# Performance work log

Measured on AMD Instinct MI355X. Metric: run time of the kernel, lower is better.

Reference implementation:

```python
import jax, jax.numpy as jnp
import numpy as np
from jax import lax

B, T, C, H, W = 1, 6, 64, 128, 128
DG, K = 16, 9          # deformable groups, 3x3 kernel positions
CG = C // DG
MRM = 10.0             # max_residue_magnitude


def _conv3(x, w, b):
    y = lax.conv_general_dilated(x, w, (1, 1), 'SAME',
                                 dimension_numbers=('NCHW', 'OIHW', 'NCHW'))
    return y + b[None, :, None, None]


def _leaky(x):
    return jnp.where(x >= 0, x, 0.1 * x)


def _bilinear(img, py, px):
    # img [N,Cc,h,w]; py/px [N,*S] unnormalized pixel coords; zero padding outside.
    N, Cc, h, w = img.shape
    S = py.shape[1:]
    py = py.reshape(N, -1)
    px = px.reshape(N, -1)
    y0 = jnp.floor(py); x0 = jnp.floor(px)
    fy = py - y0; fx = px - x0
    y0 = y0.astype(jnp.int32); x0 = x0.astype(jnp.int32)
    imf = img.reshape(N, Cc, h * w)

    def corner(yi, xi, wt):
        valid = (yi >= 0) & (yi < h) & (xi >= 0) & (xi < w)
        idx = jnp.clip(yi, 0, h - 1) * w + jnp.clip(xi, 0, w - 1)
        v = jax.vmap(lambda im, ix: im[:, ix])(imf, idx)  # [N,Cc,M]
        return v * (wt * valid)[:, None, :]

    out = (corner(y0, x0, (1 - fy) * (1 - fx))
           + corner(y0, x0 + 1, (1 - fy) * fx)
           + corner(y0 + 1, x0, fy * (1 - fx))
           + corner(y0 + 1, x0 + 1, fy * fx))
    return out.reshape(N, Cc, *S)


def _flow_warp(x, flow):
    # flow [N,2,H,W]: channel 0 = x-displacement, channel 1 = y-displacement
    gy = jnp.arange(H, dtype=jnp.float32)
    gx = jnp.arange(W, dtype=jnp.float32)
    py = gy[None, :, None] + flow[:, 1]
    px = gx[None, None, :] + flow[:, 0]
    return _bilinear(x, py, px)


def _mod_deform_conv(x, offset, mask, w, b):
    # offset [N, 2*DG*K, H, W] interleaved (y,x) per (group, kernel pos); mask [N, DG*K, H, W]
    N = x.shape[0]
    off = offset.reshape(N, DG, K, 2, H, W)
    kh = (jnp.arange(K) // 3).astype(jnp.float32)
    kw = (jnp.arange(K) % 3).astype(jnp.float32)
    gy = jnp.arange(H, dtype=jnp.float32)
    gx = jnp.arange(W, dtype=jnp.float32)
    # stride 1, padding 1, dilation 1, 3x3 kernel
    py = gy[None, None, None, :, None] - 1.0 + kh[None, None, :, None, None] + off[:, :, :, 0]
    px = gx[None, None, None, None, :] - 1.0 + kw[None, None, :, None, None] + off[:, :, :, 1]
    xg = x.reshape(N, DG, CG, H, W).reshape(N * DG, CG, H, W)
    s = _bilinear(xg, py.reshape(N * DG, K, H, W), px.reshape(N * DG, K, H, W))
    s = s.reshape(N, DG, CG, K, H, W) * mask.reshape(N, DG, 1, K, H, W)
    wr = w.reshape(C, DG, CG, K)
    return jnp.einsum('ngckhw,ogck->nohw', s, wr) + b[None, :, None, None]


def setup_inputs() -> dict:
    key = jax.random.key(0)
    ks = jax.random.split(key, 10)
    rn = lambda k, s, sc: jax.random.normal(k, s, jnp.float32) * sc
    cin = 2 * C + 2  # (1 + n_frames//2)*C + n_frames
    return {
        'x': rn(ks[0], (B, T, C, H, W), 1.0),
        'flows_backward': rn(ks[1], (B, T - 1, 2, H, W), 2.0),
        'flows_forward': rn(ks[2], (B, T - 1, 2, H, W), 2.0),
        'cw1': rn(ks[3], (C, cin, 3, 3), 1.0 / np.sqrt(cin * 9)),
        'cb1': jnp.zeros((C,), jnp.float32),
        'cw2': rn(ks[4], (C, C, 3, 3), 1.0 / np.sqrt(C * 9)),
        'cb2': jnp.zeros((C,), jnp.float32),
        'cw3': rn(ks[5], (C, C, 3, 3), 1.0 / np.sqrt(C * 9)),
        'cb3': jnp.zeros((C,), jnp.float32),
        # original zero-inits the last conv; use small random so offsets/masks are nontrivial
        'cw4': rn(ks[6], (3 * K * DG, C, 3, 3), 0.01),
        'cb4': jnp.zeros((3 * K * DG,), jnp.float32),
        'dcn_w': rn(ks[7], (C, C, 3, 3), 1.0 / np.sqrt(C * 9)),
        'dcn_b': jnp.zeros((C,), jnp.float32),
    }


def reference(x, flows_backward, flows_forward, cw1, cb1, cw2, cb2, cw3, cb3,
              cw4, cb4, dcn_w, dcn_b):
    # Batch all backward-pass frame pairs (i=T-1..1) and forward-pass pairs (i=0..T-2)
    # into one effective batch of B*2*(T-1) independent DCN calls.
    xi = jnp.concatenate([x[:, 1:], x[:, :-1]], axis=1)      # source frames
    cur = jnp.concatenate([x[:, :-1], x[:, 1:]], axis=1)     # target (current) frames
    fl = jnp.concatenate([flows_backward, flows_forward], axis=1)
    N = B * 2 * (T - 1)
    xi = xi.reshape(N, C, H, W)
    cur = cur.reshape(N, C, H, W)
    fl = fl.reshape(N, 2, H, W)

    warped = _flow_warp(xi, fl)
    inp = jnp.concatenate([warped, cur, fl], axis=1)          # [N, 2C+2, H, W]
    h1 = _leaky(_conv3(inp, cw1, cb1))
    h2 = _leaky(_conv3(h1, cw2, cb2))
    h3 = _leaky(_conv3(h2, cw3, cb3))
    out = _conv3(h3, cw4, cb4)                                # [N, 3*9*DG, H, W]
    o1, o2, m = jnp.split(out, 3, axis=1)
    offset = MRM * jnp.tanh(jnp.concatenate([o1, o2], axis=1))
    # flow.flip(1).repeat -> interleaved (fy, fx) added to every (group, kernel pos)
    offset = offset + jnp.tile(fl[:, ::-1], (1, DG * K, 1, 1))
    mask = jax.nn.sigmoid(m)

    feat = _mod_deform_conv(xi, offset, mask, dcn_w, dcn_b)   # [N, C, H, W]
    feat = feat.reshape(B, 2, T - 1, C, H, W)
    zeros = jnp.zeros((B, 1, C, H, W), feat.dtype)
    x_backward = jnp.concatenate([feat[:, 0], zeros], axis=1)  # [B, T, C, H, W]
    x_forward = jnp.concatenate([zeros, feat[:, 1]], axis=1)   # [B, T, C, H, W]
    return x_backward, x_forward
```

## Files before the change

kernel.cpp:

```cpp
#include <hip/hip_runtime.h>
#include <math.h>

#define NP   10
#define C_   64
#define H_   128
#define W_   128
#define HW   (H_*W_)
#define MRM_ 10.0f

#define OMB8_OFF 23040u
#define LDS8_TOT 30720

#define W1T_N 82944
#define W2T_N 36864
#define W4_N  294912
#define DWT_N 49152

typedef __bf16 bf16x8 __attribute__((ext_vector_type(8)));
typedef float  f32x16 __attribute__((ext_vector_type(16)));

#define MEM_FENCE() do { asm volatile("" ::: "memory"); \
                         __builtin_amdgcn_sched_barrier(0); } while (0)

__device__ __forceinline__ f32x16 mfma32(bf16x8 a, bf16x8 b, f32x16 c) {
    return __builtin_amdgcn_mfma_f32_32x32x16_bf16(a, b, c, 0, 0, 0);
}

__device__ __forceinline__ ushort bfrn(float f) {
    uint u = __builtin_bit_cast(uint, f);
    u += 0x7FFFu + ((u >> 16) & 1u);
    return (ushort)(u >> 16);
}
__device__ __forceinline__ float blo(uint u) { return __builtin_bit_cast(float, u << 16); }
__device__ __forceinline__ float bhi(uint u) { return __builtin_bit_cast(float, u & 0xFFFF0000u); }
__device__ __forceinline__ float fast_tanh(float x) {
    float e = __expf(2.f * x);
    return 1.f - 2.f / (e + 1.f);
}

__device__ __forceinline__ const float* xi_base(const float* x, int n) {
    int f = (n < 5) ? (n + 1) : (n - 5);
    return x + (size_t)f * C_ * HW;
}
__device__ __forceinline__ const float* cur_base(const float* x, int n) {
    int f = (n < 5) ? n : (n - 4);
    return x + (size_t)f * C_ * HW;
}
__device__ __forceinline__ const float* fl_base(const float* fb, const float* ff, int n) {
    return (n < 5) ? (fb + (size_t)n * 2 * HW) : (ff + (size_t)(n - 5) * 2 * HW);
}

struct Bil { int i00, i01, i10, i11; float m00, m01, m10, m11; };
__device__ __forceinline__ Bil bil(float py, float px) {
    float y0f = floorf(py), x0f = floorf(px);
    int iy0 = (int)y0f, ix0 = (int)x0f;
    float ay = py - y0f, ax = px - x0f;
    bool v0y = (unsigned)iy0 < (unsigned)H_;
    bool v1y = (unsigned)(iy0 + 1) < (unsigned)H_;
    bool v0x = (unsigned)ix0 < (unsigned)W_;
    bool v1x = (unsigned)(ix0 + 1) < (unsigned)W_;
    int cy0 = min(max(iy0, 0), H_ - 1), cy1 = min(max(iy0 + 1, 0), H_ - 1);
    int cx0 = min(max(ix0, 0), W_ - 1), cx1 = min(max(ix0 + 1, 0), W_ - 1);
    Bil r;
    r.m00 = (1.f - ay) * (1.f - ax) * (float)(v0y && v0x);
    r.m01 = (1.f - ay) * ax         * (float)(v0y && v1x);
    r.m10 = ay * (1.f - ax)         * (float)(v1y && v0x);
    r.m11 = ay * ax                 * (float)(v1y && v1x);
    r.i00 = cy0 * W_ + cx0; r.i01 = cy0 * W_ + cx1;
    r.i10 = cy1 * W_ + cx0; r.i11 = cy1 * W_ + cx1;
    return r;
}

__global__ __launch_bounds__(256) void k_prep(
        const float* __restrict__ cw1, const float* __restrict__ cw2,
        const float* __restrict__ cw3, const float* __restrict__ cw4,
        const float* __restrict__ cb4, const float* __restrict__ dw,
        ushort* __restrict__ w1t, ushort* __restrict__ w2t,
        ushort* __restrict__ w3t, ushort* __restrict__ w4t,
        ushort* __restrict__ dwtb, float* __restrict__ pb4) {
    int id = blockIdx.x * 256 + threadIdx.x;
    if (id < W1T_N) {
        int blk = id >> 9, e = id & 511;
        int c = blk / 18, r = blk % 18; int t = r >> 1, nf = r & 1;
        int l = e >> 3, j = e & 7;
        int ci = c * 16 + (l >> 5) * 8 + j;
        int oc = nf * 32 + (l & 31);
        w1t[id] = (ci < 130) ? bfrn(cw1[((size_t)oc * 130 + ci) * 9 + t]) : (ushort)0;
        return;
    }
    id -= W1T_N;
    if (id < W2T_N) {
        int blk = id >> 9, e = id & 511;
        int c = blk / 18, r = blk % 18; int t = r >> 1, nf = r & 1;
        int l = e >> 3, j = e & 7;
        int ci = c * 16 + (l >> 5) * 8 + j;
        int oc = nf * 32 + (l & 31);
        w2t[id] = bfrn(cw2[((size_t)oc * 64 + ci) * 9 + t]);
        return;
    }
    id -= W2T_N;
    if (id < W2T_N) {
        int blk = id >> 9, e = id & 511;
        int c = blk / 18, r = blk % 18; int t = r >> 1, nf = r & 1;
        int l = e >> 3, j = e & 7;
        int ci = c * 16 + (l >> 5) * 8 + j;
        int oc = nf * 32 + (l & 31);
        w3t[id] = bfrn(cw3[((size_t)oc * 64 + ci) * 9 + t]);
        return;
    }
    id -= W2T_N;
    if (id < W4_N) {
        int blk = id >> 9, e = id & 511;
        int c = blk / 144, r = blk - c * 144;
        int t = r >> 4, g = r & 15;
        int l = e >> 3, j = e & 7;
        int nn = l & 31, kh = l >> 5;
        int ci = c * 16 + kh * 8 + j;
        int ch = (nn < 18) ? g * 18 + nn : (nn < 27 ? 288 + g * 9 + (nn - 18) : -1);
        float v = (ch >= 0) ? cw4[((size_t)ch * 64 + ci) * 9 + t] : 0.f;
        w4t[id] = bfrn(v);
        return;
    }
    id -= W4_N;
    if (id < DWT_N) {
        int blk = id >> 9, e = id & 511;
        int g = blk / 6, r = blk - g * 6;
        int kst = r >> 1, nf = r & 1;
        int l = e >> 3, j = e & 7;
        int kk = kst * 16 + (l >> 5) * 8 + j;
        int oc = nf * 32 + (l & 31);
        float v = (kk < 36) ? dw[((size_t)oc * 64 + g * 4 + (kk & 3)) * 9 + (kk >> 2)] : 0.f;
        dwtb[id] = bfrn(v);
        return;
    }
    id -= DWT_N;
    if (id < 512) {
        int g = id >> 5, nn = id & 31;
        int ch = (nn < 18) ? g * 18 + nn : (nn < 27 ? 288 + g * 9 + (nn - 18) : -1);
        pb4[id] = (ch >= 0) ? cb4[ch] : 0.f;
    }
}

__global__ __launch_bounds__(256) void k_warp(
        const float* __restrict__ x, const float* __restrict__ fb,
        const float* __restrict__ ff, ushort* __restrict__ warped) {
    int gid = blockIdx.x * 256 + threadIdx.x;
    int n = gid / HW, pos = gid % HW;
    int y = pos / W_, xx = pos % W_;
    const float* fl = fl_base(fb, ff, n);
    float fx = fl[pos], fy = fl[HW + pos];
    Bil b = bil((float)y + fy, (float)xx + fx);
    const float* xb = xi_base(x, n);
    ushort* wout = warped + (size_t)n * C_ * HW + pos;
    for (int c = 0; c < C_; ++c) {
        const float* p = xb + c * HW;
        wout[c * HW] = bfrn(b.m00 * p[b.i00] + b.m01 * p[b.i01]
                          + b.m10 * p[b.i10] + b.m11 * p[b.i11]);
    }
}

__global__ __launch_bounds__(256) void k_xt(
        const float* __restrict__ x, ushort* __restrict__ xt) {
    int gid = blockIdx.x * 256 + threadIdx.x;
    int f = gid / HW, pos = gid % HW;
    const float* src = x + (size_t)f * C_ * HW + pos;
    ushort* dst = xt + (size_t)f * 16 * HW * 4;
    #pragma unroll
    for (int g = 0; g < 16; ++g) {
        uint2 v;
        ushort h0 = bfrn(src[(g * 4 + 0) * HW]);
        ushort h1 = bfrn(src[(g * 4 + 1) * HW]);
        ushort h2 = bfrn(src[(g * 4 + 2) * HW]);
        ushort h3 = bfrn(src[(g * 4 + 3) * HW]);
        v.x = (uint)h0 | ((uint)h1 << 16);
        v.y = (uint)h2 | ((uint)h3 << 16);
        *(uint2*)(dst + ((size_t)g * HW + pos) * 4) = v;
    }
}

template<int NCHUNK, int SRC>
__global__ __launch_bounds__(256, 3) void k_convm(
        const ushort* __restrict__ inb, const float* __restrict__ x,
        const float* __restrict__ fb, const float* __restrict__ ff,
        const ushort* __restrict__ wt, const float* __restrict__ bias,
        ushort* __restrict__ outp) {
    __shared__ __align__(16) char ldsb[41472];
    int tid = threadIdx.x;
    int lane = tid & 63, w = tid >> 6;
    int id = (blockIdx.x & 7) * 80 + (blockIdx.x >> 3);
    int bx = id & 7, by = (id >> 3) & 7, n = id >> 6;
    int col = lane & 31, khalf = lane >> 5;

    const float* flp = fl_base(fb, ff, n);
    const float* curp = cur_base(x, n);

    f32x16 acc[2][2];
    #pragma unroll
    for (int a = 0; a < 2; ++a)
        #pragma unroll
        for (int b = 0; b < 2; ++b)
            #pragma unroll
            for (int r = 0; r < 16; ++r) acc[a][b][r] = 0.f;

    int xb2 = col & 15;
    int rb0 = 4 * w + ((col >> 4) & 1);
    const int NPASS = (NCHUNK + 3) / 4;

    #pragma unroll
    for (int p = 0; p < NPASS; ++p) {
        const int c0 = 4 * p;
        const int cN = (NCHUNK - c0 >= 4) ? 4 : (NCHUNK - c0);
        __syncthreads();
        for (int cc = 0; cc < cN; ++cc) {
            int chunk = c0 + cc;
            int cbase = chunk * 16 + w * 4;
            for (int v = 0; v < 6; ++v) {
                int cell = v * 64 + lane;
                if (cell < 324) {
                    int cy = cell / 18, cx = cell - cy * 18;
                    int gy = by * 16 + cy - 1, gx = bx * 16 + cx - 1;
                    bool ok = ((unsigned)gy < 128u) && ((unsigned)gx < 128u);
                    int pos = gy * W_ + gx;
                    uint2 hv; hv.x = hv.y = 0;
                    if (SRC == 1 || chunk < 4) {
                        const ushort* sp = inb + ((size_t)n * 64 + cbase) * HW + pos;
                        ushort h0 = ok ? sp[0] : (ushort)0;
                        ushort h1 = ok ? sp[HW] : (ushort)0;
                        ushort h2 = ok ? sp[2 * HW] : (ushort)0;
                        ushort h3 = ok ? sp[3 * HW] : (ushort)0;
                        hv.x = (uint)h0 | ((uint)h1 << 16);
                        hv.y = (uint)h2 | ((uint)h3 << 16);
                    } else if (chunk < 8) {
                        const float* sp = curp + (size_t)(cbase - 64) * HW + pos;
                        ushort h0 = bfrn(ok ? sp[0] : 0.f);
                        ushort h1 = bfrn(ok ? sp[HW] : 0.f);
                        ushort h2 = bfrn(ok ? sp[2 * HW] : 0.f);
                        ushort h3 = bfrn(ok ? sp[3 * HW] : 0.f);
                        hv.x = (uint)h0 | ((uint)h1 << 16);
                        hv.y = (uint)h2 | ((uint)h3 << 16);
                    } else {
                        float v0 = 0.f, v1 = 0.f;
                        if (w == 0 && ok) { v0 = flp[pos]; v1 = flp[HW + pos]; }
                        hv.x = (uint)bfrn(v0) | ((uint)bfrn(v1) << 16);
                    }
                    uint byte = (uint)cell * 128 + (uint)cc * 32 + (uint)w * 8;
                    byte ^= ((uint)(cell & 7)) << 4;
                    *(uint2*)(ldsb + byte) = hv;
                }
            }
        }
        __syncthreads();
        for (int cc = 0; cc < cN; ++cc) {
            #pragma unroll
            for (int t = 0; t < 9; ++t) {
                const int ky = t / 3, kx = t % 3;
                size_t bb = (size_t)(((c0 + cc) * 9 + t) * 2) * 512 + (size_t)lane * 8;
                bf16x8 b0 = *(const bf16x8*)(wt + bb);
                bf16x8 b1 = *(const bf16x8*)(wt + bb + 512);
                #pragma unroll
                for (int f = 0; f < 2; ++f) {
                    int cell = (rb0 + 2 * f + ky) * 18 + xb2 + kx;
                    uint byte = (uint)cell * 128 + (uint)(2 * cc + khalf) * 16;
                    byte ^= ((uint)(cell & 7)) << 4;
                    bf16x8 a = *(const bf16x8*)(ldsb + byte);
                    acc[f][0] = mfma32(a, b0, acc[f][0]);
                    acc[f][1] = mfma32(a, b1, acc[f][1]);
                }
            }
        }
    }

    ushort* op = outp + (size_t)n * 64 * HW;
    #pragma unroll
    for (int f = 0; f < 2; ++f)
        #pragma unroll
        for (int nf = 0; nf < 2; ++nf) {
            int oc = nf * 32 + col;
            float bs = bias[oc];
            #pragma unroll
            for (int r = 0; r < 16; ++r) {
                int pxl = 64 * w + 32 * f + (r & 3) + 8 * (r >> 2) + 4 * khalf;
                int y = by * 16 + (pxl >> 4), xx = bx * 16 + (pxl & 15);
                float v = acc[f][nf][r] + bs;
                v = (v >= 0.f) ? v : 0.1f * v;
                op[(size_t)oc * HW + y * W_ + xx] = bfrn(v);
            }
        }
}

__global__ __launch_bounds__(128, 2) void k_dcn11(
        const ushort* __restrict__ h3, const ushort* __restrict__ xt,
        const float* __restrict__ fb, const float* __restrict__ ff,
        const ushort* __restrict__ w4hi,
        const ushort* __restrict__ dwtb, const float* __restrict__ pb4,
        const float* __restrict__ db, float* __restrict__ outb) {
    __shared__ __align__(16) char lds[LDS8_TOT];
    _Float16* OMBH = (_Float16*)(lds + OMB8_OFF);

    int tid = threadIdx.x;
    int lane = tid & 63, w = tid >> 6;
    int id = (blockIdx.x & 7) * 160 + (blockIdx.x >> 3);
    int bx = id & 15, by = (id >> 4) & 7, n = id >> 7;
    int col = lane & 31, khalf = lane >> 5;

    const ushort* h3n = h3 + (size_t)n * 64 * HW;
    const float* fl = fl_base(fb, ff, n);
    int fxi = (n < 5) ? (n + 1) : (n - 5);
    const ushort* xtn = xt + (size_t)fxi * 16 * HW * 4;

    int Yp = by * 16 + (tid >> 3), Xp = bx * 8 + (tid & 7);
    float fxr = fl[Yp * W_ + Xp];
    float fyr = fl[HW + Yp * W_ + Xp];

    for (int c = 0; c < 4; ++c) {
        for (int v = 0; v < 3; ++v) {
            int cell = v * 64 + lane;
            if (cell < 180) {
                int cy = cell / 10, cx = cell - cy * 10;
                int gy = by * 16 + cy - 1, gx = bx * 8 + cx - 1;
                bool ok = ((unsigned)gy < 128u) && ((unsigned)gx < 128u);
                const ushort* srcp = h3n + (size_t)(c * 16 + w * 8) * HW + gy * W_ + gx;
                uint2 hv0, hv1;
                ushort q0 = ok ? srcp[0] : (ushort)0;
                ushort q1 = ok ? srcp[HW] : (ushort)0;
                ushort q2 = ok ? srcp[2 * HW] : (ushort)0;
                ushort q3 = ok ? srcp[3 * HW] : (ushort)0;
                ushort q4 = ok ? srcp[4 * HW] : (ushort)0;
                ushort q5 = ok ? srcp[5 * HW] : (ushort)0;
                ushort q6 = ok ? srcp[6 * HW] : (ushort)0;
                ushort q7 = ok ? srcp[7 * HW] : (ushort)0;
                hv0.x = (uint)q0 | ((uint)q1 << 16);
                hv0.y = (uint)q2 | ((uint)q3 << 16);
                hv1.x = (uint)q4 | ((uint)q5 << 16);
                hv1.y = (uint)q6 | ((uint)q7 << 16);
                uint byte = (uint)cell * 128 + (uint)c * 32 + (uint)w * 16;
                byte ^= ((uint)(cell & 7)) << 4;
                *(uint2*)(lds + byte) = hv0;
                *(uint2*)(lds + byte + 8) = hv1;
            }
        }
    }
    __syncthreads();

    f32x16 zero16;
    #pragma unroll
    for (int r = 0; r < 16; ++r) zero16[r] = 0.f;

    f32x16 cd[2][2];
    #pragma unroll
    for (int a = 0; a < 2; ++a)
        #pragma unroll
        for (int b = 0; b < 2; ++b) cd[a][b] = zero16;

    int colq = col >> 3;
    int colx = col & 7;
    int ad0 = (lane & 31) * 4;

    for (int sp = 0; sp < 8; ++sp) {
        int g0 = sp * 2;
        f32x16 c4[2][2];
        #pragma unroll
        for (int a = 0; a < 2; ++a)
            #pragma unroll
            for (int b = 0; b < 2; ++b) c4[a][b] = zero16;

        __builtin_amdgcn_s_setprio(1);
        #pragma unroll 1
        for (int c = 0; c < 4; ++c) {
            #pragma unroll
            for (int t = 0; t < 9; ++t) {
                const int ky = t / 3, kx = t % 3;
                size_t bb = (size_t)((c * 9 + t) * 16) * 512 + (size_t)lane * 8;
                bf16x8 bh0 = *(const bf16x8*)(w4hi + bb + (size_t)g0 * 512);
                bf16x8 bh1 = *(const bf16x8*)(w4hi + bb + (size_t)(g0 + 1) * 512);
                #pragma unroll
                for (int f = 0; f < 2; ++f) {
                    int cell = (8 * w + 4 * f + colq + ky) * 10 + colx + kx;
                    uint byte = (uint)cell * 128 + (uint)(2 * c + khalf) * 16;
                    byte ^= ((uint)(cell & 7)) << 4;
                    bf16x8 ah = *(const bf16x8*)(lds + byte);
                    c4[0][f] = mfma32(ah, bh0, c4[0][f]);
                    c4[1][f] = mfma32(ah, bh1, c4[1][f]);
                }
            }
        }
        __builtin_amdgcn_s_setprio(0);

        #pragma unroll
        for (int gg = 0; gg < 2; ++gg) {
            int g = g0 + gg;
            MEM_FENCE();
            if (col < 27) {
                float pb = pb4[g * 32 + col];
                #pragma unroll
                for (int f = 0; f < 2; ++f)
                    #pragma unroll
                    for (int r = 0; r < 16; ++r) {
                        int pxl = 64 * w + 32 * f + (r & 3) + 8 * (r >> 2) + 4 * khalf;
                        float v = c4[gg][f][r] + pb;
                        v = (col < 18) ? MRM_ * fast_tanh(v) : 1.f / (1.f + __expf(-v));
                        OMBH[pxl * 30 + col] = (_Float16)v;
                    }
            }
            MEM_FENCE();
            int pkx[9], pky[9];
            {
                int px = tid;
                float Yf = (float)Yp, Xf = (float)Xp;
                const ushort* xg = xtn + (size_t)g * HW * 4;
                #pragma unroll
                for (int k = 0; k < 9; ++k) {
                    float oy = (float)OMBH[px * 30 + 2 * k] + fyr;
                    float ox = (float)OMBH[px * 30 + 2 * k + 1] + fxr;
                    float mk = (float)OMBH[px * 30 + 18 + k];
                    Bil b = bil(Yf - 1.f + (float)(k / 3) + oy,
                                Xf - 1.f + (float)(k % 3) + ox);
                    uint2 q00 = *(const uint2*)(xg + (size_t)b.i00 * 4);
                    uint2 q01 = *(const uint2*)(xg + (size_t)b.i01 * 4);
                    uint2 q10 = *(const uint2*)(xg + (size_t)b.i10 * 4);
                    uint2 q11 = *(const uint2*)(xg + (size_t)b.i11 * 4);
                    float s0 = b.m00 * blo(q00.x) + b.m01 * blo(q01.x)
                             + b.m10 * blo(q10.x) + b.m11 * blo(q11.x);
                    float s1 = b.m00 * bhi(q00.x) + b.m01 * bhi(q01.x)
                             + b.m10 * bhi(q10.x) + b.m11 * bhi(q11.x);
                    float s2 = b.m00 * blo(q00.y) + b.m01 * blo(q01.y)
                             + b.m10 * blo(q10.y) + b.m11 * blo(q11.y);
                    float s3 = b.m00 * bhi(q00.y) + b.m01 * bhi(q01.y)
                             + b.m10 * bhi(q10.y) + b.m11 * bhi(q11.y);
                    pkx[k] = (int)((uint)bfrn(s0 * mk) | ((uint)bfrn(s1 * mk) << 16));
                    pky[k] = (int)((uint)bfrn(s2 * mk) | ((uint)bfrn(s3 * mk) << 16));
                }
            }
            __builtin_amdgcn_s_setprio(1);
            #pragma unroll
            for (int kst = 0; kst < 3; ++kst) {
                size_t dbb = (size_t)((g * 3 + kst) * 2) * 512 + (size_t)lane * 8;
                bf16x8 b0 = *(const bf16x8*)(dwtb + dbb);
                bf16x8 b1 = *(const bf16x8*)(dwtb + dbb + 512);
                #pragma unroll
                for (int f = 0; f < 2; ++f) {
                    int ad = ad0 + f * 128;
                    uint a0, a1, a2, a3;
                    if (kst < 2) {
                        const int t0 = kst * 4;
                        uint x0 = (uint)__builtin_amdgcn_ds_bpermute(ad, pkx[t0]);
                        uint y0 = (uint)__builtin_amdgcn_ds_bpermute(ad, pky[t0]);
                        uint x1 = (uint)__builtin_amdgcn_ds_bpermute(ad, pkx[t0 + 1]);
                        uint y1 = (uint)__builtin_amdgcn_ds_bpermute(ad, pky[t0 + 1]);
                        uint x2 = (uint)__builtin_amdgcn_ds_bpermute(ad, pkx[t0 + 2]);
                        uint y2 = (uint)__builtin_amdgcn_ds_bpermute(ad, pky[t0 + 2]);
                        uint x3 = (uint)__builtin_amdgcn_ds_bpermute(ad, pkx[t0 + 3]);
                        uint y3 = (uint)__builtin_amdgcn_ds_bpermute(ad, pky[t0 + 3]);
                        a0 = khalf ? x2 : x0;
                        a1 = khalf ? y2 : y0;
                        a2 = khalf ? x3 : x1;
                        a3 = khalf ? y3 : y1;
                    } else {
                        uint x8 = (uint)__builtin_amdgcn_ds_bpermute(ad, pkx[8]);
                        uint y8 = (uint)__builtin_amdgcn_ds_bpermute(ad, pky[8]);
                        a0 = khalf ? 0u : x8;
                        a1 = khalf ? 0u : y8;
                        a2 = 0u; a3 = 0u;
                    }
                    uint4 av; av.x = a0; av.y = a1; av.z = a2; av.w = a3;
                    bf16x8 a = __builtin_bit_cast(bf16x8, av);
                    cd[f][0] = mfma32(a, b0, cd[f][0]);
                    cd[f][1] = mfma32(a, b1, cd[f][1]);
                }
            }
            __builtin_amdgcn_s_setprio(0);
        }
    }

    float* base = (n < 5) ? outb + (size_t)n * 64 * HW
                          : outb + (size_t)(n + 2) * 64 * HW;
    #pragma unroll
    for (int f = 0; f < 2; ++f)
        #pragma unroll
        for (int nf = 0; nf < 2; ++nf) {
            int oc = nf * 32 + col;
            float bias = db[oc];
            #pragma unroll
            for (int r = 0; r < 16; ++r) {
                int pxl = 64 * w + 32 * f + (r & 3) + 8 * (r >> 2) + 4 * khalf;
                int y = by * 16 + (pxl >> 3), xx = bx * 8 + (pxl & 7);
                base[(size_t)oc * HW + y * W_ + xx] = cd[f][nf][r] + bias;
            }
        }
}

extern "C" void kernel_launch(void* const* d_in, const int* in_sizes, int n_in,
                              void* d_out, int out_size, void* d_ws, size_t ws_size,
                              hipStream_t stream) {
    (void)in_sizes; (void)n_in; (void)out_size; (void)ws_size;
    const float* x   = (const float*)d_in[0];
    const float* fb  = (const float*)d_in[1];
    const float* ff  = (const float*)d_in[2];
    const float* cw1 = (const float*)d_in[3];
    const float* cb1 = (const float*)d_in[4];
    const float* cw2 = (const float*)d_in[5];
    const float* cb2 = (const float*)d_in[6];
    const float* cw3 = (const float*)d_in[7];
    const float* cb3 = (const float*)d_in[8];
    const float* cw4 = (const float*)d_in[9];
    const float* cb4 = (const float*)d_in[10];
    const float* dw  = (const float*)d_in[11];
    const float* db  = (const float*)d_in[12];
    float* out = (float*)d_out;

    ushort* h1b  = (ushort*)d_ws;
    ushort* h3b  = h1b + 10485760;
    ushort* w1t  = h3b + 10485760;
    ushort* w2t  = w1t + W1T_N;
    ushort* w3t  = w2t + W2T_N;
    ushort* w4t  = w3t + W2T_N;
    ushort* dwtb = w4t + W4_N;
    float*  pb4  = (float*)(dwtb + DWT_N);
    ushort* xtb  = h1b;
    ushort* wpb  = (ushort*)d_out;
    ushort* h2b  = wpb + 10485760;

    k_prep<<<1958, 256, 0, stream>>>(cw1, cw2, cw3, cw4, cb4, dw,
                                     w1t, w2t, w3t, w4t, dwtb, pb4);
    k_warp<<<(NP * HW) / 256, 256, 0, stream>>>(x, fb, ff, wpb);
    k_convm<9, 0><<<640, 256, 0, stream>>>(wpb, x, fb, ff, w1t, cb1, h1b);
    k_convm<4, 1><<<640, 256, 0, stream>>>(h1b, x, fb, ff, w2t, cb2, h2b);
    k_xt<<<(6 * HW) / 256, 256, 0, stream>>>(x, xtb);
    k_convm<4, 1><<<640, 256, 0, stream>>>(h2b, x, fb, ff, w3t, cb3, h3b);

    hipMemsetAsync((char*)d_out + (size_t)5 * C_ * HW * sizeof(float), 0, (size_t)C_ * HW * sizeof(float), stream);
    hipMemsetAsync((char*)d_out + (size_t)6 * C_ * HW * sizeof(float), 0, (size_t)C_ * HW * sizeof(float), stream);

    k_dcn11<<<1280, 128, 0, stream>>>(h3b, xtb, fb, ff, w4t, dwtb, pb4, db, out);
}
```

Before: 604.1 us.

## Halve DCN tile to 8x8 pixels per block, split bilinear taps across half-waves

The fused offset-conv plus deformable-conv kernel now processes an 8x8 pixel tile per 128-thread block instead of 16x8. That halves the accumulator registers and shrinks LDS to 16KB, and launch bounds are raised to 5 blocks per SIMD with twice as many blocks launched. Bilinear sampling is split between the two 32-lane halves of each wave: each lane computes 5 taps instead of 9, and the results are redistributed with ds_bpermute to build the MFMA A operands. In exchange, the halo overhead of the h3 tile load goes up and the conv4 weight loads are amortised over fewer pixels.

```diff
diff --git a/kernel.cpp b/kernel.cpp
--- a/kernel.cpp
+++ b/kernel.cpp
@@ -8,8 +8,8 @@
 #define HW   (H_*W_)
 #define MRM_ 10.0f
 
-#define OMB8_OFF 23040u
-#define LDS8_TOT 30720
+#define OMB13_OFF 12800u
+#define LDS13_TOT 16384
 
 #define W1T_N 82944
 #define W2T_N 36864
@@ -288,19 +288,19 @@
         }
 }
 
-__global__ __launch_bounds__(128, 2) void k_dcn11(
+__global__ __launch_bounds__(128, 5) void k_dcn13(
         const ushort* __restrict__ h3, const ushort* __restrict__ xt,
         const float* __restrict__ fb, const float* __restrict__ ff,
         const ushort* __restrict__ w4hi,
         const ushort* __restrict__ dwtb, const float* __restrict__ pb4,
         const float* __restrict__ db, float* __restrict__ outb) {
-    __shared__ __align__(16) char lds[LDS8_TOT];
-    _Float16* OMBH = (_Float16*)(lds + OMB8_OFF);
+    __shared__ __align__(16) char lds[LDS13_TOT];
+    _Float16* OMBH = (_Float16*)(lds + OMB13_OFF);
 
     int tid = threadIdx.x;
     int lane = tid & 63, w = tid >> 6;
-    int id = (blockIdx.x & 7) * 160 + (blockIdx.x >> 3);
-    int bx = id & 15, by = (id >> 4) & 7, n = id >> 7;
+    int id = (blockIdx.x & 7) * 320 + (blockIdx.x >> 3);
+    int bx = id & 15, by = (id >> 4) & 15, n = id >> 8;
     int col = lane & 31, khalf = lane >> 5;
 
     const ushort* h3n = h3 + (size_t)n * 64 * HW;
@@ -308,36 +308,34 @@
     int fxi = (n < 5) ? (n + 1) : (n - 5);
     const ushort* xtn = xt + (size_t)fxi * 16 * HW * 4;
 
-    int Yp = by * 16 + (tid >> 3), Xp = bx * 8 + (tid & 7);
+    int Yp = by * 8 + 4 * w + (col >> 3), Xp = bx * 8 + (col & 7);
     float fxr = fl[Yp * W_ + Xp];
     float fyr = fl[HW + Yp * W_ + Xp];
 
     for (int c = 0; c < 4; ++c) {
-        for (int v = 0; v < 3; ++v) {
-            int cell = v * 64 + lane;
-            if (cell < 180) {
-                int cy = cell / 10, cx = cell - cy * 10;
-                int gy = by * 16 + cy - 1, gx = bx * 8 + cx - 1;
-                bool ok = ((unsigned)gy < 128u) && ((unsigned)gx < 128u);
-                const ushort* srcp = h3n + (size_t)(c * 16 + w * 8) * HW + gy * W_ + gx;
-                uint2 hv0, hv1;
-                ushort q0 = ok ? srcp[0] : (ushort)0;
-                ushort q1 = ok ? srcp[HW] : (ushort)0;
-                ushort q2 = ok ? srcp[2 * HW] : (ushort)0;
-                ushort q3 = ok ? srcp[3 * HW] : (ushort)0;
-                ushort q4 = ok ? srcp[4 * HW] : (ushort)0;
-                ushort q5 = ok ? srcp[5 * HW] : (ushort)0;
-                ushort q6 = ok ? srcp[6 * HW] : (ushort)0;
-                ushort q7 = ok ? srcp[7 * HW] : (ushort)0;
-                hv0.x = (uint)q0 | ((uint)q1 << 16);
-                hv0.y = (uint)q2 | ((uint)q3 << 16);
-                hv1.x = (uint)q4 | ((uint)q5 << 16);
-                hv1.y = (uint)q6 | ((uint)q7 << 16);
-                uint byte = (uint)cell * 128 + (uint)c * 32 + (uint)w * 16;
-                byte ^= ((uint)(cell & 7)) << 4;
-                *(uint2*)(lds + byte) = hv0;
-                *(uint2*)(lds + byte + 8) = hv1;
-            }
+        for (int task = tid; task < 200; task += 128) {
+            int cell = task >> 1, half = task & 1;
+            int cy = cell / 10, cx = cell - cy * 10;
+            int gy = by * 8 + cy - 1, gx = bx * 8 + cx - 1;
+            bool ok = ((unsigned)gy < 128u) && ((unsigned)gx < 128u);
+            const ushort* srcp = h3n + (size_t)(c * 16 + half * 8) * HW + gy * W_ + gx;
+            uint2 hv0, hv1;
+            ushort q0 = ok ? srcp[0] : (ushort)0;
+            ushort q1 = ok ? srcp[HW] : (ushort)0;
+            ushort q2 = ok ? srcp[2 * HW] : (ushort)0;
+            ushort q3 = ok ? srcp[3 * HW] : (ushort)0;
+            ushort q4 = ok ? srcp[4 * HW] : (ushort)0;
+            ushort q5 = ok ? srcp[5 * HW] : (ushort)0;
+            ushort q6 = ok ? srcp[6 * HW] : (ushort)0;
+            ushort q7 = ok ? srcp[7 * HW] : (ushort)0;
+            hv0.x = (uint)q0 | ((uint)q1 << 16);
+            hv0.y = (uint)q2 | ((uint)q3 << 16);
+            hv1.x = (uint)q4 | ((uint)q5 << 16);
+            hv1.y = (uint)q6 | ((uint)q7 << 16);
+            uint byte = (uint)cell * 128 + (uint)c * 32 + (uint)half * 16;
+            byte ^= ((uint)(cell & 7)) << 4;
+            *(uint2*)(lds + byte) = hv0;
+            *(uint2*)(lds + byte + 8) = hv1;
         }
     }
     __syncthreads();
@@ -346,26 +344,21 @@
     #pragma unroll
     for (int r = 0; r < 16; ++r) zero16[r] = 0.f;
 
-    f32x16 cd[2][2];
-    #pragma unroll
-    for (int a = 0; a < 2; ++a)
-        #pragma unroll
-        for (int b = 0; b < 2; ++b) cd[a][b] = zero16;
+    f32x16 cd[2];
+    cd[0] = zero16; cd[1] = zero16;
 
     int colq = col >> 3;
     int colx = col & 7;
-    int ad0 = (lane & 31) * 4;
+    int ad_lo = col * 4;
+    int ad_hi = ad_lo + 128;
 
     for (int sp = 0; sp < 8; ++sp) {
         int g0 = sp * 2;
-        f32x16 c4[2][2];
-        #pragma unroll
-        for (int a = 0; a < 2; ++a)
-            #pragma unroll
-            for (int b = 0; b < 2; ++b) c4[a][b] = zero16;
+        f32x16 c4[2];
+        c4[0] = zero16; c4[1] = zero16;
 
         __builtin_amdgcn_s_setprio(1);
-        #pragma unroll 1
+        #pragma unroll 2
         for (int c = 0; c < 4; ++c) {
             #pragma unroll
             for (int t = 0; t < 9; ++t) {
@@ -373,15 +366,12 @@
                 size_t bb = (size_t)((c * 9 + t) * 16) * 512 + (size_t)lane * 8;
                 bf16x8 bh0 = *(const bf16x8*)(w4hi + bb + (size_t)g0 * 512);
                 bf16x8 bh1 = *(const bf16x8*)(w4hi + bb + (size_t)(g0 + 1) * 512);
-                #pragma unroll
-                for (int f = 0; f < 2; ++f) {
-                    int cell = (8 * w + 4 * f + colq + ky) * 10 + colx + kx;
-                    uint byte = (uint)cell * 128 + (uint)(2 * c + khalf) * 16;
-                    byte ^= ((uint)(cell & 7)) << 4;
-                    bf16x8 ah = *(const bf16x8*)(lds + byte);
-                    c4[0][f] = mfma32(ah, bh0, c4[0][f]);
-                    c4[1][f] = mfma32(ah, bh1, c4[1][f]);
-                }
+                int cell = (4 * w + colq + ky) * 10 + colx + kx;
+                uint byte = (uint)cell * 128 + (uint)(2 * c + khalf) * 16;
+                byte ^= ((uint)(cell & 7)) << 4;
+                bf16x8 ah = *(const bf16x8*)(lds + byte);
+                c4[0] = mfma32(ah, bh0, c4[0]);
+                c4[1] = mfma32(ah, bh1, c4[1]);
             }
         }
         __builtin_amdgcn_s_setprio(0);
@@ -393,80 +383,102 @@
             if (col < 27) {
                 float pb = pb4[g * 32 + col];
                 #pragma unroll
-                for (int f = 0; f < 2; ++f)
-                    #pragma unroll
-                    for (int r = 0; r < 16; ++r) {
-                        int pxl = 64 * w + 32 * f + (r & 3) + 8 * (r >> 2) + 4 * khalf;
-                        float v = c4[gg][f][r] + pb;
-                        v = (col < 18) ? MRM_ * fast_tanh(v) : 1.f / (1.f + __expf(-v));
-                        OMBH[pxl * 30 + col] = (_Float16)v;
-                    }
+                for (int r = 0; r < 16; ++r) {
+                    int pxw = (r & 3) + 8 * (r >> 2) + 4 * khalf;
+                    float v = c4[gg][r] + pb;
+                    v = (col < 18) ? MRM_ * fast_tanh(v) : 1.f / (1.f + __expf(-v));
+                    OMBH[(32 * w + pxw) * 28 + col] = (_Float16)v;
+                }
             }
             MEM_FENCE();
-            int pkx[9], pky[9];
+            int pkx[5], pky[5];
             {
-                int px = tid;
                 float Yf = (float)Yp, Xf = (float)Xp;
                 const ushort* xg = xtn + (size_t)g * HW * 4;
+                const _Float16* op = OMBH + (32 * w + col) * 28;
                 #pragma unroll
-                for (int k = 0; k < 9; ++k) {
-                    float oy = (float)OMBH[px * 30 + 2 * k] + fyr;
-                    float ox = (float)OMBH[px * 30 + 2 * k + 1] + fxr;
-                    float mk = (float)OMBH[px * 30 + 18 + k];
-                    Bil b = bil(Yf - 1.f + (float)(k / 3) + oy,
-                                Xf - 1.f + (float)(k % 3) + ox);
-                    uint2 q00 = *(const uint2*)(xg + (size_t)b.i00 * 4);
-                    uint2 q01 = *(const uint2*)(xg + (size_t)b.i01 * 4);
-                    uint2 q10 = *(const uint2*)(xg + (size_t)b.i10 * 4);
-                    uint2 q11 = *(const uint2*)(xg + (size_t)b.i11 * 4);
-                    float s0 = b.m00 * blo(q00.x) + b.m01 * blo(q01.x)
-                             + b.m10 * blo(q10.x) + b.m11 * blo(q11.x);
-                    float s1 = b.m00 * bhi(q00.x) + b.m01 * bhi(q01.x)
-                             + b.m10 * bhi(q10.x) + b.m11 * bhi(q11.x);
-                    float s2 = b.m00 * blo(q00.y) + b.m01 * blo(q01.y)
-                             + b.m10 * blo(q10.y) + b.m11 * blo(q11.y);
-                    float s3 = b.m00 * bhi(q00.y) + b.m01 * bhi(q01.y)
-                             + b.m10 * bhi(q10.y) + b.m11 * bhi(q11.y);
-                    pkx[k] = (int)((uint)bfrn(s0 * mk) | ((uint)bfrn(s1 * mk) << 16));
-                    pky[k] = (int)((uint)bfrn(s2 * mk) | ((uint)bfrn(s3 * mk) << 16));
+                for (int k = 0; k < 5; ++k) {
+                    if (k == 4 && lane >= 32) { pkx[4] = 0; pky[4] = 0; }
+                    else {
+                        int tap = (lane < 32) ? k : 5 + k;
+                        float oy = (float)op[2 * tap] + fyr;
+                        float ox = (float)op[2 * tap + 1] + fxr;
+                        float mk = (float)op[18 + tap];
+                        Bil b = bil(Yf - 1.f + (float)(tap / 3) + oy,
+                                    Xf - 1.f + (float)(tap % 3) + ox);
+                        uint2 q00 = *(const uint2*)(xg + (size_t)b.i00 * 4);
+                        uint2 q01 = *(const uint2*)(xg + (size_t)b.i01 * 4);
+                        uint2 q10 = *(const uint2*)(xg + (size_t)b.i10 * 4);
+                        uint2 q11 = *(const uint2*)(xg + (size_t)b.i11 * 4);
+                        float s0 = b.m00 * blo(q00.x) + b.m01 * blo(q01.x)
+                                 + b.m10 * blo(q10.x) + b.m11 * blo(q11.x);
+                        float s1 = b.m00 * bhi(q00.x) + b.m01 * bhi(q01.x)
+                                 + b.m10 * bhi(q10.x) + b.m11 * bhi(q11.x);
+                        float s2 = b.m00 * blo(q00.y) + b.m01 * blo(q01.y)
+                                 + b.m10 * blo(q10.y) + b.m11 * blo(q11.y);
+                        float s3 = b.m00 * bhi(q00.y) + b.m01 * bhi(q01.y)
+                                 + b.m10 * bhi(q10.y) + b.m11 * bhi(q11.y);
+                        pkx[k] = (int)((uint)bfrn(s0 * mk) | ((uint)bfrn(s1 * mk) << 16));
+                        pky[k] = (int)((uint)bfrn(s2 * mk) | ((uint)bfrn(s3 * mk) << 16));
+                    }
                 }
             }
             __builtin_amdgcn_s_setprio(1);
-            #pragma unroll
-            for (int kst = 0; kst < 3; ++kst) {
-                size_t dbb = (size_t)((g * 3 + kst) * 2) * 512 + (size_t)lane * 8;
+            {
+                size_t dbb = (size_t)((g * 3 + 0) * 2) * 512 + (size_t)lane * 8;
                 bf16x8 b0 = *(const bf16x8*)(dwtb + dbb);
                 bf16x8 b1 = *(const bf16x8*)(dwtb + dbb + 512);
-                #pragma unroll
-                for (int f = 0; f < 2; ++f) {
-                    int ad = ad0 + f * 128;
-                    uint a0, a1, a2, a3;
-                    if (kst < 2) {
-                        const int t0 = kst * 4;
-                        uint x0 = (uint)__builtin_amdgcn_ds_bpermute(ad, pkx[t0]);
-                        uint y0 = (uint)__builtin_amdgcn_ds_bpermute(ad, pky[t0]);
-                        uint x1 = (uint)__builtin_amdgcn_ds_bpermute(ad, pkx[t0 + 1]);
-                        uint y1 = (uint)__builtin_amdgcn_ds_bpermute(ad, pky[t0 + 1]);
-                        uint x2 = (uint)__builtin_amdgcn_ds_bpermute(ad, pkx[t0 + 2]);
-                        uint y2 = (uint)__builtin_amdgcn_ds_bpermute(ad, pky[t0 + 2]);
-                        uint x3 = (uint)__builtin_amdgcn_ds_bpermute(ad, pkx[t0 + 3]);
-                        uint y3 = (uint)__builtin_amdgcn_ds_bpermute(ad, pky[t0 + 3]);
-                        a0 = khalf ? x2 : x0;
-                        a1 = khalf ? y2 : y0;
-                        a2 = khalf ? x3 : x1;
-                        a3 = khalf ? y3 : y1;
-                    } else {
-                        uint x8 = (uint)__builtin_amdgcn_ds_bpermute(ad, pkx[8]);
-                        uint y8 = (uint)__builtin_amdgcn_ds_bpermute(ad, pky[8]);
-                        a0 = khalf ? 0u : x8;
-                        a1 = khalf ? 0u : y8;
-                        a2 = 0u; a3 = 0u;
-                    }
-                    uint4 av; av.x = a0; av.y = a1; av.z = a2; av.w = a3;
-                    bf16x8 a = __builtin_bit_cast(bf16x8, av);
-                    cd[f][0] = mfma32(a, b0, cd[f][0]);
-                    cd[f][1] = mfma32(a, b1, cd[f][1]);
-                }
+                uint x0 = (uint)__builtin_amdgcn_ds_bpermute(ad_lo, pkx[0]);
+                uint y0 = (uint)__builtin_amdgcn_ds_bpermute(ad_lo, pky[0]);
+                uint x1 = (uint)__builtin_amdgcn_ds_bpermute(ad_lo, pkx[1]);
+                uint y1 = (uint)__builtin_amdgcn_ds_bpermute(ad_lo, pky[1]);
+                uint x2 = (uint)__builtin_amdgcn_ds_bpermute(ad_lo, pkx[2]);
+                uint y2 = (uint)__builtin_amdgcn_ds_bpermute(ad_lo, pky[2]);
+                uint x3 = (uint)__builtin_amdgcn_ds_bpermute(ad_lo, pkx[3]);
+                uint y3 = (uint)__builtin_amdgcn_ds_bpermute(ad_lo, pky[3]);
+                uint4 av;
+                av.x = khalf ? x2 : x0;
+                av.y = khalf ? y2 : y0;
+                av.z = khalf ? x3 : x1;
+                av.w = khalf ? y3 : y1;
+                bf16x8 a = __builtin_bit_cast(bf16x8, av);
+                cd[0] = mfma32(a, b0, cd[0]);
+                cd[1] = mfma32(a, b1, cd[1]);
+            }
+            {
+                size_t dbb = (size_t)((g * 3 + 1) * 2) * 512 + (size_t)lane * 8;
+                bf16x8 b0 = *(const bf16x8*)(dwtb + dbb);
+                bf16x8 b1 = *(const bf16x8*)(dwtb + dbb + 512);
+                uint x4 = (uint)__builtin_amdgcn_ds_bpermute(ad_lo, pkx[4]);
+                uint y4 = (uint)__builtin_amdgcn_ds_bpermute(ad_lo, pky[4]);
+                uint x5 = (uint)__builtin_amdgcn_ds_bpermute(ad_hi, pkx[0]);
+                uint y5 = (uint)__builtin_amdgcn_ds_bpermute(ad_hi, pky[0]);
+                uint x6 = (uint)__builtin_amdgcn_ds_bpermute(ad_hi, pkx[1]);
+                uint y6 = (uint)__builtin_amdgcn_ds_bpermute(ad_hi, pky[1]);
+                uint x7 = (uint)__builtin_amdgcn_ds_bpermute(ad_hi, pkx[2]);
+                uint y7 = (uint)__builtin_amdgcn_ds_bpermute(ad_hi, pky[2]);
+                uint4 av;
+                av.x = khalf ? x6 : x4;
+                av.y = khalf ? y6 : y4;
+                av.z = khalf ? x7 : x5;
+                av.w = khalf ? y7 : y5;
+                bf16x8 a = __builtin_bit_cast(bf16x8, av);
+                cd[0] = mfma32(a, b0, cd[0]);
+                cd[1] = mfma32(a, b1, cd[1]);
+            }
+            {
+                size_t dbb = (size_t)((g * 3 + 2) * 2) * 512 + (size_t)lane * 8;
+                bf16x8 b0 = *(const bf16x8*)(dwtb + dbb);
+                bf16x8 b1 = *(const bf16x8*)(dwtb + dbb + 512);
+                uint x8 = (uint)__builtin_amdgcn_ds_bpermute(ad_hi, pkx[3]);
+                uint y8 = (uint)__builtin_amdgcn_ds_bpermute(ad_hi, pky[3]);
+                uint4 av;
+                av.x = khalf ? 0u : x8;
+                av.y = khalf ? 0u : y8;
+                av.z = 0u; av.w = 0u;
+                bf16x8 a = __builtin_bit_cast(bf16x8, av);
+                cd[0] = mfma32(a, b0, cd[0]);
+                cd[1] = mfma32(a, b1, cd[1]);
             }
             __builtin_amdgcn_s_setprio(0);
         }
@@ -475,18 +487,16 @@
     float* base = (n < 5) ? outb + (size_t)n * 64 * HW
                           : outb + (size_t)(n + 2) * 64 * HW;
     #pragma unroll
-    for (int f = 0; f < 2; ++f)
+    for (int nf = 0; nf < 2; ++nf) {
+        int oc = nf * 32 + col;
+        float bias = db[oc];
         #pragma unroll
-        for (int nf = 0; nf < 2; ++nf) {
-            int oc = nf * 32 + col;
-            float bias = db[oc];
-            #pragma unroll
-            for (int r = 0; r < 16; ++r) {
-                int pxl = 64 * w + 32 * f + (r & 3) + 8 * (r >> 2) + 4 * khalf;
-                int y = by * 16 + (pxl >> 3), xx = bx * 8 + (pxl & 7);
-                base[(size_t)oc * HW + y * W_ + xx] = cd[f][nf][r] + bias;
-            }
-        }
+        for (int r = 0; r < 16; ++r) {
+            int pxw = (r & 3) + 8 * (r >> 2) + 4 * khalf;
+            int y = by * 8 + 4 * w + (pxw >> 3), xx = bx * 8 + (pxw & 7);
+            base[(size_t)oc * HW + y * W_ + xx] = cd[nf][r] + bias;
+        }
+    }
 }
 
 extern "C" void kernel_launch(void* const* d_in, const int* in_sizes, int n_in,
@@ -531,5 +541,5 @@
     hipMemsetAsync((char*)d_out + (size_t)5 * C_ * HW * sizeof(float), 0, (size_t)C_ * HW * sizeof(float), stream);
     hipMemsetAsync((char*)d_out + (size_t)6 * C_ * HW * sizeof(float), 0, (size_t)C_ * HW * sizeof(float), stream);
 
-    k_dcn11<<<1280, 128, 0, stream>>>(h3b, xtb, fb, ff, w4t, dwtb, pb4, db, out);
-}
+    k_dcn13<<<2560, 128, 0, stream>>>(h3b, xtb, fb, ff, w4t, dwtb, pb4, db, out);
+}
```

Result: slower. 819.0 us (+35.6%).
